# Kernel optimization log

Measured on AMD Instinct MI355X. Metric: run time of the kernel, lower is better.

The kernel has to match this reference:

```python
import jax, jax.numpy as jnp
import numpy as np

B, N, C, G = 8, 4096, 768, 16
D = C // G  # per-group channel dim = 48


def setup_inputs() -> dict:
    key = jax.random.key(0)
    ks = jax.random.split(key, 5)
    s = 1.0 / np.sqrt(C)
    return {
        "x": jax.random.normal(ks[0], (B, N, C), dtype=jnp.float32),
        "w_qkv": jax.random.normal(ks[1], (C, 3 * C), dtype=jnp.float32) * s,
        "b_qkv": jnp.zeros((3 * C,), dtype=jnp.float32),
        "w_proj": jax.random.normal(ks[2], (C, C), dtype=jnp.float32) * s,
        "b_proj": jnp.zeros((C,), dtype=jnp.float32),
    }


def reference(x, w_qkv, b_qkv, w_proj, b_proj):
    Bx, Nx, Cx = x.shape
    g, d = G, Cx // G
    qkv = x @ w_qkv + b_qkv                      # [B, N, 3C]
    qkv = qkv.reshape(Bx, Nx, 3, g, d)
    qkv = jnp.transpose(qkv, (2, 0, 3, 1, 4))    # [3, B, g, N, d]
    q, k, v = qkv[0], qkv[1], qkv[2]
    q = q * (float(Nx) ** -0.5)
    # channel attention: contract over tokens -> [B, g, d, d]
    attn = jnp.einsum("bgnd,bgne->bgde", q, k)
    attn = jax.nn.softmax(attn, axis=-1)
    # out = attn @ v^T -> [B, g, d, N], then back to [B, N, C]
    out = jnp.einsum("bgde,bgne->bgnd", attn, v)  # [B, g, N, d]
    out = jnp.transpose(out, (0, 2, 1, 3)).reshape(Bx, Nx, Cx)
    return out @ w_proj + b_proj
```

## Files before the change

### kernel.cpp

```cpp
#include <hip/hip_runtime.h>
#include <stdint.h>


using short8 = __attribute__((__ext_vector_type__(8))) short;
using f32x4  = __attribute__((__ext_vector_type__(4))) float;

typedef const void __attribute__((address_space(1))) gv_t;
typedef void __attribute__((address_space(3))) lv_t;

__device__ __forceinline__ void gll16(const void* g, void* l) {
  __builtin_amdgcn_global_load_lds((gv_t*)g, (lv_t*)l, 16, 0, 0);
}

__device__ __forceinline__ uint16_t f2b(float f) {
  uint32_t x = __float_as_uint(f);
  uint32_t r = (x + 0x7fffu + ((x >> 16) & 1u)) >> 16;
  return (uint16_t)r;
}
__device__ __forceinline__ float b2f(uint16_t u) {
  return __uint_as_float(((uint32_t)u) << 16);
}


__global__ __launch_bounds__(256) void cast_x_kernel(const float* __restrict__ x,
                                                     uint16_t* __restrict__ xb, int n4) {
  int i = blockIdx.x * 256 + threadIdx.x;
  if (i >= n4) return;
  f32x4 v = ((const f32x4*)x)[i];
  union { uint16_t u[4]; uint64_t q; } o;
  o.u[0] = f2b(v[0]); o.u[1] = f2b(v[1]); o.u[2] = f2b(v[2]); o.u[3] = f2b(v[3]);
  ((uint64_t*)xb)[i] = o.q;
}

__global__ __launch_bounds__(256) void transpose_cast_kernel(const float* __restrict__ w,
                                                             uint16_t* __restrict__ wt,
                                                             int K, int N) {
  int i = blockIdx.x * 256 + threadIdx.x;
  if (i >= N * K) return;
  int n = i / K, k = i - n * K;
  wt[i] = f2b(w[(size_t)k * N + n]);
}


template<int MODE>
__global__ __launch_bounds__(256, 1) void gemm256_kernel(
    const uint16_t* __restrict__ A, const uint16_t* __restrict__ Bt,
    const float* __restrict__ bias,
    uint16_t* __restrict__ Qb, uint16_t* __restrict__ Kb,
    uint16_t* __restrict__ Vb, float* __restrict__ outf) {
  constexpr int NT = 24;
  constexpr int NB = (MODE == 0) ? 9 : 3;
  constexpr int NWG = 256 * NB;
  constexpr int CPX = NWG / 8;
  __shared__ uint16_t lds[3 * 12288];

  const int tid  = threadIdx.x;
  const int lane = tid & 63, w = tid >> 6;
  const int lrow = lane & 15, kb = lane >> 4;

  int wg = (int)blockIdx.x;
  wg = (wg & 7) * CPX + (wg >> 3);
  const int mblk = wg / NB, nblk = wg % NB;
  const int m0 = mblk * 128, n0 = nblk * 256;
  const bool sw = (MODE == 0) && (n0 < 1536);

  const int grow  = lane >> 2;
  const int gslot = ((lane & 3) ^ ((lane >> 3) & 3)) << 3;
  const size_t arow0 = (size_t)(m0 + w * 32 + grow) * 768 + gslot;
  const size_t brow0 = (size_t)(n0 + w * 64 + grow) * 768 + gslot;

  auto stage = [&](int ts, int sl) {
    const size_t ko = (size_t)ts * 32;
    uint16_t* la = lds + sl * 12288 + w * 1024;
    uint16_t* lb = lds + sl * 12288 + 4096 + w * 2048;
    gll16(A  + arow0 + ko,            la);
    gll16(A  + arow0 + ko + 16 * 768, la + 512);
    gll16(Bt + brow0 + ko,            lb);
    gll16(Bt + brow0 + ko + 16 * 768, lb + 512);
    gll16(Bt + brow0 + ko + 32 * 768, lb + 1024);
    gll16(Bt + brow0 + ko + 48 * 768, lb + 1536);
  };

  const int xslot = (kb ^ ((lrow >> 1) & 3)) << 3;

  f32x4 acc[8][4] = {};

  stage(0, 0); stage(1, 1);
  asm volatile("s_waitcnt vmcnt(6)" ::: "memory");
  __builtin_amdgcn_s_barrier();
  __builtin_amdgcn_sched_barrier(0);

  int sl = 0;
  for (int t = 0; t < NT; ++t) {
    const int sl2 = (sl == 0) ? 2 : sl - 1;
    if (t + 2 < NT) stage(t + 2, sl2);
    const uint16_t* sa = lds + sl * 12288;
    const uint16_t* sb = sa + 4096;
    short8 av[8], bv4[4];
#pragma unroll
    for (int mf = 0; mf < 8; ++mf)
      av[mf] = *(const short8*)(sa + (mf * 16 + lrow) * 32 + xslot);
#pragma unroll
    for (int nf = 0; nf < 4; ++nf)
      bv4[nf] = *(const short8*)(sb + (w * 64 + nf * 16 + lrow) * 32 + xslot);
    __builtin_amdgcn_s_setprio(1);
    if (sw) {
#pragma unroll
      for (int mf = 0; mf < 8; ++mf)
#pragma unroll
        for (int nf = 0; nf < 4; ++nf)
          acc[mf][nf] = __builtin_amdgcn_mfma_f32_16x16x32_bf16(bv4[nf], av[mf], acc[mf][nf], 0, 0, 0);
    } else {
#pragma unroll
      for (int mf = 0; mf < 8; ++mf)
#pragma unroll
        for (int nf = 0; nf < 4; ++nf)
          acc[mf][nf] = __builtin_amdgcn_mfma_f32_16x16x32_bf16(av[mf], bv4[nf], acc[mf][nf], 0, 0, 0);
    }
    __builtin_amdgcn_s_setprio(0);
    if (t < NT - 1) {
      if (t == NT - 2) asm volatile("s_waitcnt vmcnt(0)" ::: "memory");
      else             asm volatile("s_waitcnt vmcnt(6)" ::: "memory");
      __builtin_amdgcn_s_barrier();
      __builtin_amdgcn_sched_barrier(0);
    }
    sl = (sl == 2) ? 0 : sl + 1;
  }

  const float qscale = 0.015625f;
  if (MODE == 0) {
    const int which = n0 / 768;
    if (which < 2) {
      uint16_t* dst = (which == 0) ? Qb : Kb;
      const float sc = (which == 0) ? qscale : 1.0f;
#pragma unroll
      for (int mf = 0; mf < 8; ++mf) {
        const int token = m0 + mf * 16 + lrow;
        const int b = token >> 12, nn = token & 4095;
#pragma unroll
        for (int nf = 0; nf < 4; ++nf) {
          const int colb = n0 + w * 64 + nf * 16 + kb * 4;
#pragma unroll
          for (int r = 0; r < 4; ++r) {
            const int chan = colb + r - which * 768;
            const int g = chan / 48, d = chan - g * 48;
            dst[(((size_t)b * 16 + g) * 48 + d) * 4096 + nn] =
                f2b((acc[mf][nf][r] + bias[colb + r]) * sc);
          }
        }
      }
    } else {
#pragma unroll
      for (int mf = 0; mf < 8; ++mf) {
        const int rowb = m0 + mf * 16 + kb * 4;
#pragma unroll
        for (int nf = 0; nf < 4; ++nf) {
          const int col = n0 + w * 64 + nf * 16 + lrow;
          const int c = col - 1536, g = c / 48, d = c - g * 48;
          const float bb = bias[col];
#pragma unroll
          for (int r = 0; r < 4; ++r) {
            const int row = rowb + r;
            const int b = row >> 12, nn = row & 4095;
            Vb[(((size_t)b * 16 + g) * 4096 + nn) * 48 + d] = f2b(acc[mf][nf][r] + bb);
          }
        }
      }
    }
  } else {
#pragma unroll
    for (int mf = 0; mf < 8; ++mf) {
      const int rowb = m0 + mf * 16 + kb * 4;
#pragma unroll
      for (int nf = 0; nf < 4; ++nf) {
        const int col = n0 + w * 64 + nf * 16 + lrow;
        const float bb = bias[col];
#pragma unroll
        for (int r = 0; r < 4; ++r)
          outf[(size_t)(rowb + r) * 768 + col] = acc[mf][nf][r] + bb;
      }
    }
  }
}


__global__ __launch_bounds__(256) void logits_mfma_kernel(
    const uint16_t* __restrict__ Qt, const uint16_t* __restrict__ Kt,
    float* __restrict__ part) {
  const int bg = blockIdx.x;
  const int ch = blockIdx.y;
  const int tid = threadIdx.x;
  const int lane = tid & 63, w = tid >> 6;
  const int lrow = lane & 15, kb = lane >> 4;

  const size_t qbase = (size_t)bg * 48 * 4096;
  const int tok0 = ch * 512 + w * 128;

  f32x4 acc[3][3] = {};
#pragma unroll
  for (int s = 0; s < 4; ++s) {
    const int tok = tok0 + s * 32 + kb * 8;
    short8 av[3], bvv[3];
#pragma unroll
    for (int dm = 0; dm < 3; ++dm) {
      av[dm]  = *(const short8*)(Qt + qbase + (size_t)(dm * 16 + lrow) * 4096 + tok);
      bvv[dm] = *(const short8*)(Kt + qbase + (size_t)(dm * 16 + lrow) * 4096 + tok);
    }
#pragma unroll
    for (int dm = 0; dm < 3; ++dm)
#pragma unroll
      for (int em = 0; em < 3; ++em)
        acc[dm][em] = __builtin_amdgcn_mfma_f32_16x16x32_bf16(av[dm], bvv[em], acc[dm][em], 0, 0, 0);
  }

  __shared__ float red[4][2304];
#pragma unroll
  for (int dm = 0; dm < 3; ++dm)
#pragma unroll
    for (int em = 0; em < 3; ++em)
#pragma unroll
      for (int r = 0; r < 4; ++r) {
        const int d = dm * 16 + kb * 4 + r;
        const int e = em * 16 + lrow;
        red[w][d * 48 + e] = acc[dm][em][r];
      }
  __syncthreads();
  float* dst = part + ((size_t)ch * 128 + bg) * 2304;
  for (int i = tid; i < 2304; i += 256)
    dst[i] = red[0][i] + red[1][i] + red[2][i] + red[3][i];
}


__global__ __launch_bounds__(256) void softmax_kernel(const float* __restrict__ part,
                                                      float* __restrict__ attn) {
  const int bg = blockIdx.x;
  const int tid = threadIdx.x;
  __shared__ float l[2304];
  for (int p = tid; p < 2304; p += 256) {
    float s = 0.f;
    for (int chk = 0; chk < 8; ++chk) s += part[((size_t)chk * 128 + bg) * 2304 + p];
    l[p] = s;
  }
  __syncthreads();
  if (tid < 48) {
    const int d = tid;
    float m = -1e30f;
    for (int e = 0; e < 48; ++e) m = fmaxf(m, l[d * 48 + e]);
    float s = 0.f;
    for (int e = 0; e < 48; ++e) s += expf(l[d * 48 + e] - m);
    const float inv = 1.0f / s;
    for (int e = 0; e < 48; ++e)
      attn[(size_t)bg * 2304 + d * 48 + e] = expf(l[d * 48 + e] - m) * inv;
  }
}


__global__ __launch_bounds__(256) void blockdiag_kernel(const uint16_t* __restrict__ Vb,
                                                        const float* __restrict__ attn,
                                                        uint16_t* __restrict__ ao) {
  const int bg = blockIdx.x, ch = blockIdx.y;
  const int b = bg >> 4, g = bg & 15;
  const int tid = threadIdx.x;
  __shared__ uint16_t vs[128 * 64];
  __shared__ uint16_t as2[48 * 64];
  const size_t vbase = ((size_t)bg * 4096 + (size_t)ch * 128) * 48;
  for (int i = tid; i < 128 * 64; i += 256) {
    int n = i >> 6, e = i & 63;
    vs[i] = (e < 48) ? Vb[vbase + n * 48 + e] : (uint16_t)0;
  }
  const float* ab = attn + (size_t)bg * 2304;
  for (int i = tid; i < 48 * 64; i += 256) {
    int d = i >> 6, e = i & 63;
    as2[i] = (e < 48) ? f2b(ab[d * 48 + e]) : (uint16_t)0;
  }
  __syncthreads();
  const int lane = tid & 63, w = tid >> 6;
  const int lrow = lane & 15, kb = lane >> 4;
  f32x4 acc[2][3] = {};
#pragma unroll
  for (int ksb = 0; ksb < 2; ++ksb) {
    short8 a[2], bb[3];
#pragma unroll
    for (int i = 0; i < 2; ++i)
      a[i] = *(const short8*)(vs + (w * 32 + i * 16 + lrow) * 64 + ksb * 32 + kb * 8);
#pragma unroll
    for (int c = 0; c < 3; ++c)
      bb[c] = *(const short8*)(as2 + (c * 16 + lrow) * 64 + ksb * 32 + kb * 8);
#pragma unroll
    for (int i = 0; i < 2; ++i)
#pragma unroll
      for (int c = 0; c < 3; ++c)
        acc[i][c] = __builtin_amdgcn_mfma_f32_16x16x32_bf16(a[i], bb[c], acc[i][c], 0, 0, 0);
  }
#pragma unroll
  for (int i = 0; i < 2; ++i)
#pragma unroll
    for (int c = 0; c < 3; ++c)
#pragma unroll
      for (int r = 0; r < 4; ++r) {
        const int nl = w * 32 + i * 16 + kb * 4 + r;
        const int dcol = c * 16 + lrow;
        const size_t row = (size_t)b * 4096 + (size_t)ch * 128 + nl;
        ao[row * 768 + g * 48 + dcol] = f2b(acc[i][c][r]);
      }
}


extern "C" void kernel_launch(void* const* d_in, const int* in_sizes, int n_in,
                              void* d_out, int out_size, void* d_ws, size_t ws_size,
                              hipStream_t stream) {
  const float* x      = (const float*)d_in[0];
  const float* w_qkv  = (const float*)d_in[1];
  const float* b_qkv  = (const float*)d_in[2];
  const float* w_proj = (const float*)d_in[3];
  const float* b_proj = (const float*)d_in[4];
  float* out = (float*)d_out;

  char* w = (char*)d_ws;
  uint16_t* xb  = (uint16_t*)w; w += (size_t)32768 * 768 * 2;
  uint16_t* wqT = (uint16_t*)w; w += (size_t)2304 * 768 * 2;
  uint16_t* wpT = (uint16_t*)w; w += (size_t)768 * 768 * 2;
  uint16_t* Qt  = (uint16_t*)w; w += (size_t)128 * 48 * 4096 * 2;
  uint16_t* Kt  = (uint16_t*)w; w += (size_t)128 * 48 * 4096 * 2;
  uint16_t* Vb  = (uint16_t*)w; w += (size_t)128 * 4096 * 48 * 2;
  float* part   = (float*)w;    w += (size_t)8 * 128 * 2304 * 4;
  float* attn   = (float*)w;    w += (size_t)128 * 2304 * 4;
  uint16_t* ao  = xb;

  cast_x_kernel<<<24576, 256, 0, stream>>>(x, xb, 6291456);
  transpose_cast_kernel<<<6912, 256, 0, stream>>>(w_qkv, wqT, 768, 2304);
  transpose_cast_kernel<<<2304, 256, 0, stream>>>(w_proj, wpT, 768, 768);
  gemm256_kernel<0><<<2304, 256, 0, stream>>>(xb, wqT, b_qkv, Qt, Kt, Vb, nullptr);
  logits_mfma_kernel<<<dim3(128, 8), 256, 0, stream>>>(Qt, Kt, part);
  softmax_kernel<<<128, 256, 0, stream>>>(part, attn);
  blockdiag_kernel<<<dim3(128, 32), 256, 0, stream>>>(Vb, attn, ao);
  gemm256_kernel<1><<<768, 256, 0, stream>>>(ao, wpT, b_proj, nullptr, nullptr, nullptr, out);
}
```

Baseline: 431.9 us.

## Shrink GEMM tiles to 128x128 with 2x2 wave grid and vectorize V staging

Both projection GEMMs move from a 128x256 tile (each wave covering all 128 rows and 64 columns) to a 128x128 tile split across a 2x2 grid of waves. This halves LDS use and the accumulator registers and drops the one-block-per-SIMD launch bound, which allows more resident blocks and twice as many workgroups. In exchange each block reuses less data per K step, so more A/B traffic goes through LDS and global memory. Separately, blockdiag now loads V into shared memory with 16-byte vector loads and zero-fills the padding columns, replacing the per-element scalar copy.

```diff
diff --git a/kernel.cpp b/kernel.cpp
--- a/kernel.cpp
+++ b/kernel.cpp
@@ -43,84 +43,83 @@
 
 
 template<int MODE>
-__global__ __launch_bounds__(256, 1) void gemm256_kernel(
+__global__ __launch_bounds__(256) void gemm_ring_kernel(
     const uint16_t* __restrict__ A, const uint16_t* __restrict__ Bt,
     const float* __restrict__ bias,
     uint16_t* __restrict__ Qb, uint16_t* __restrict__ Kb,
     uint16_t* __restrict__ Vb, float* __restrict__ outf) {
   constexpr int NT = 24;
-  constexpr int NB = (MODE == 0) ? 9 : 3;
+  constexpr int NB = (MODE == 0) ? 18 : 6;
   constexpr int NWG = 256 * NB;
   constexpr int CPX = NWG / 8;
-  __shared__ uint16_t lds[3 * 12288];
+  __shared__ uint16_t lds[3 * 8192];
 
   const int tid  = threadIdx.x;
   const int lane = tid & 63, w = tid >> 6;
+  const int wm = w >> 1, wn = w & 1;
   const int lrow = lane & 15, kb = lane >> 4;
 
   int wg = (int)blockIdx.x;
   wg = (wg & 7) * CPX + (wg >> 3);
   const int mblk = wg / NB, nblk = wg % NB;
-  const int m0 = mblk * 128, n0 = nblk * 256;
+  const int m0 = mblk * 128, n0 = nblk * 128;
   const bool sw = (MODE == 0) && (n0 < 1536);
 
   const int grow  = lane >> 2;
   const int gslot = ((lane & 3) ^ ((lane >> 3) & 3)) << 3;
   const size_t arow0 = (size_t)(m0 + w * 32 + grow) * 768 + gslot;
-  const size_t brow0 = (size_t)(n0 + w * 64 + grow) * 768 + gslot;
+  const size_t brow0 = (size_t)(n0 + w * 32 + grow) * 768 + gslot;
 
   auto stage = [&](int ts, int sl) {
     const size_t ko = (size_t)ts * 32;
-    uint16_t* la = lds + sl * 12288 + w * 1024;
-    uint16_t* lb = lds + sl * 12288 + 4096 + w * 2048;
+    uint16_t* la = lds + sl * 8192 + w * 1024;
+    uint16_t* lb = lds + sl * 8192 + 4096 + w * 1024;
     gll16(A  + arow0 + ko,            la);
     gll16(A  + arow0 + ko + 16 * 768, la + 512);
     gll16(Bt + brow0 + ko,            lb);
     gll16(Bt + brow0 + ko + 16 * 768, lb + 512);
-    gll16(Bt + brow0 + ko + 32 * 768, lb + 1024);
-    gll16(Bt + brow0 + ko + 48 * 768, lb + 1536);
   };
 
   const int xslot = (kb ^ ((lrow >> 1) & 3)) << 3;
 
-  f32x4 acc[8][4] = {};
+  f32x4 acc[4][4] = {};
 
   stage(0, 0); stage(1, 1);
-  asm volatile("s_waitcnt vmcnt(6)" ::: "memory");
+  asm volatile("s_waitcnt vmcnt(4)" ::: "memory");
   __builtin_amdgcn_s_barrier();
   __builtin_amdgcn_sched_barrier(0);
 
   int sl = 0;
   for (int t = 0; t < NT; ++t) {
-    const int sl2 = (sl == 0) ? 2 : sl - 1;
+    const int sl2 = (sl >= 1) ? sl - 1 : 2;
     if (t + 2 < NT) stage(t + 2, sl2);
-    const uint16_t* sa = lds + sl * 12288;
+    const uint16_t* sa = lds + sl * 8192;
     const uint16_t* sb = sa + 4096;
-    short8 av[8], bv4[4];
-#pragma unroll
-    for (int mf = 0; mf < 8; ++mf)
-      av[mf] = *(const short8*)(sa + (mf * 16 + lrow) * 32 + xslot);
+    short8 av[4], bv4[4];
+#pragma unroll
+    for (int mf = 0; mf < 4; ++mf)
+      av[mf] = *(const short8*)(sa + (wm * 64 + mf * 16 + lrow) * 32 + xslot);
 #pragma unroll
     for (int nf = 0; nf < 4; ++nf)
-      bv4[nf] = *(const short8*)(sb + (w * 64 + nf * 16 + lrow) * 32 + xslot);
+      bv4[nf] = *(const short8*)(sb + (wn * 64 + nf * 16 + lrow) * 32 + xslot);
     __builtin_amdgcn_s_setprio(1);
     if (sw) {
 #pragma unroll
-      for (int mf = 0; mf < 8; ++mf)
+      for (int mf = 0; mf < 4; ++mf)
 #pragma unroll
         for (int nf = 0; nf < 4; ++nf)
           acc[mf][nf] = __builtin_amdgcn_mfma_f32_16x16x32_bf16(bv4[nf], av[mf], acc[mf][nf], 0, 0, 0);
     } else {
 #pragma unroll
-      for (int mf = 0; mf < 8; ++mf)
+      for (int mf = 0; mf < 4; ++mf)
 #pragma unroll
         for (int nf = 0; nf < 4; ++nf)
           acc[mf][nf] = __builtin_amdgcn_mfma_f32_16x16x32_bf16(av[mf], bv4[nf], acc[mf][nf], 0, 0, 0);
     }
     __builtin_amdgcn_s_setprio(0);
     if (t < NT - 1) {
-      if (t == NT - 2) asm volatile("s_waitcnt vmcnt(0)" ::: "memory");
-      else             asm volatile("s_waitcnt vmcnt(6)" ::: "memory");
+      if (t < NT - 2) asm volatile("s_waitcnt vmcnt(4)" ::: "memory");
+      else            asm volatile("s_waitcnt vmcnt(0)" ::: "memory");
       __builtin_amdgcn_s_barrier();
       __builtin_amdgcn_sched_barrier(0);
     }
@@ -134,12 +133,12 @@
       uint16_t* dst = (which == 0) ? Qb : Kb;
       const float sc = (which == 0) ? qscale : 1.0f;
 #pragma unroll
-      for (int mf = 0; mf < 8; ++mf) {
-        const int token = m0 + mf * 16 + lrow;
+      for (int mf = 0; mf < 4; ++mf) {
+        const int token = m0 + wm * 64 + mf * 16 + lrow;
         const int b = token >> 12, nn = token & 4095;
 #pragma unroll
         for (int nf = 0; nf < 4; ++nf) {
-          const int colb = n0 + w * 64 + nf * 16 + kb * 4;
+          const int colb = n0 + wn * 64 + nf * 16 + kb * 4;
 #pragma unroll
           for (int r = 0; r < 4; ++r) {
             const int chan = colb + r - which * 768;
@@ -151,11 +150,11 @@
       }
     } else {
 #pragma unroll
-      for (int mf = 0; mf < 8; ++mf) {
-        const int rowb = m0 + mf * 16 + kb * 4;
+      for (int mf = 0; mf < 4; ++mf) {
+        const int rowb = m0 + wm * 64 + mf * 16 + kb * 4;
 #pragma unroll
         for (int nf = 0; nf < 4; ++nf) {
-          const int col = n0 + w * 64 + nf * 16 + lrow;
+          const int col = n0 + wn * 64 + nf * 16 + lrow;
           const int c = col - 1536, g = c / 48, d = c - g * 48;
           const float bb = bias[col];
 #pragma unroll
@@ -169,11 +168,11 @@
     }
   } else {
 #pragma unroll
-    for (int mf = 0; mf < 8; ++mf) {
-      const int rowb = m0 + mf * 16 + kb * 4;
+    for (int mf = 0; mf < 4; ++mf) {
+      const int rowb = m0 + wm * 64 + mf * 16 + kb * 4;
 #pragma unroll
       for (int nf = 0; nf < 4; ++nf) {
-        const int col = n0 + w * 64 + nf * 16 + lrow;
+        const int col = n0 + wn * 64 + nf * 16 + lrow;
         const float bb = bias[col];
 #pragma unroll
         for (int r = 0; r < 4; ++r)
@@ -264,9 +263,15 @@
   __shared__ uint16_t vs[128 * 64];
   __shared__ uint16_t as2[48 * 64];
   const size_t vbase = ((size_t)bg * 4096 + (size_t)ch * 128) * 48;
-  for (int i = tid; i < 128 * 64; i += 256) {
-    int n = i >> 6, e = i & 63;
-    vs[i] = (e < 48) ? Vb[vbase + n * 48 + e] : (uint16_t)0;
+  const uint4* vg = (const uint4*)(Vb + vbase);
+  for (int u = tid; u < 768; u += 256) {
+    const int n = u / 6, c = u - n * 6;
+    *(uint4*)(vs + n * 64 + c * 8) = vg[u];
+  }
+  {
+    const int n = tid >> 1, c = 6 + (tid & 1);
+    uint4 z; z.x = z.y = z.z = z.w = 0u;
+    *(uint4*)(vs + n * 64 + c * 8) = z;
   }
   const float* ab = attn + (size_t)bg * 2304;
   for (int i = tid; i < 48 * 64; i += 256) {
@@ -330,9 +335,9 @@
   cast_x_kernel<<<24576, 256, 0, stream>>>(x, xb, 6291456);
   transpose_cast_kernel<<<6912, 256, 0, stream>>>(w_qkv, wqT, 768, 2304);
   transpose_cast_kernel<<<2304, 256, 0, stream>>>(w_proj, wpT, 768, 768);
-  gemm256_kernel<0><<<2304, 256, 0, stream>>>(xb, wqT, b_qkv, Qt, Kt, Vb, nullptr);
+  gemm_ring_kernel<0><<<4608, 256, 0, stream>>>(xb, wqT, b_qkv, Qt, Kt, Vb, nullptr);
   logits_mfma_kernel<<<dim3(128, 8), 256, 0, stream>>>(Qt, Kt, part);
   softmax_kernel<<<128, 256, 0, stream>>>(part, attn);
   blockdiag_kernel<<<dim3(128, 32), 256, 0, stream>>>(Vb, attn, ao);
-  gemm256_kernel<1><<<768, 256, 0, stream>>>(ao, wpT, b_proj, nullptr, nullptr, nullptr, out);
-}
+  gemm_ring_kernel<1><<<1536, 256, 0, stream>>>(ao, wpT, b_proj, nullptr, nullptr, nullptr, out);
+}
```

After: 402.5 us. -6.8%, faster.
